# Optimization experiments

Measured on AMD Instinct MI355X. Metric: run time of the kernel, lower is better.

The kernel has to match this reference:

```python
import jax, jax.numpy as jnp
import numpy as np

DIM = 2048
N_HEAD = 16
HEAD_DIM = DIM // N_HEAD


def setup_inputs() -> dict:
    key = jax.random.key(0)
    ks = jax.random.split(key, 7)
    B, N = 2, 2048
    s = 1.0 / np.sqrt(DIM)
    return {
        "x": jax.random.normal(ks[0], (B, N, DIM), dtype=jnp.float32),
        "Wq": jax.random.normal(ks[1], (DIM, DIM), dtype=jnp.float32) * s,
        "bq": jnp.zeros((DIM,), dtype=jnp.float32),
        "Wkv": jax.random.normal(ks[2], (DIM, 2 * HEAD_DIM), dtype=jnp.float32) * s,
        "bkv": jnp.zeros((2 * HEAD_DIM,), dtype=jnp.float32),
        "Wo": jax.random.normal(ks[3], (DIM, DIM), dtype=jnp.float32) * s,
        "bo": jnp.zeros((DIM,), dtype=jnp.float32),
    }


def reference(x, Wq, bq, Wkv, bkv, Wo, bo):
    B, N, D = x.shape
    # Q projection -> (B, H, N, hd)
    q = (x @ Wq + bq).reshape(B, N, N_HEAD, HEAD_DIM).transpose(0, 2, 1, 3)
    # shared single-head K/V (kv = x, self-attention path)
    kvp = x @ Wkv + bkv  # (B, M, 2*hd)
    k, v = kvp[..., :HEAD_DIM], kvp[..., HEAD_DIM:]  # (B, M, hd) each
    scale = 1.0 / np.sqrt(HEAD_DIM).astype(np.float32)
    # broadcast shared K over heads without materializing expanded K/V
    scores = jnp.einsum("bhnd,bmd->bhnm", q, k) * scale  # (B, H, N, M)
    attn = jax.nn.softmax(scores, axis=-1)
    out = jnp.einsum("bhnm,bmd->bhnd", attn, v)  # (B, H, N, hd)
    out = out.transpose(0, 2, 1, 3).reshape(B, N, D)
    return out @ Wo + bo
```

## Files before the change

### kernel.cpp

```cpp
#include <hip/hip_runtime.h>
#include <math.h>

using bf16x8 = __attribute__((ext_vector_type(8))) short;
using f32x4  = __attribute__((ext_vector_type(4))) float;
using f32x16 = __attribute__((ext_vector_type(16))) float;
using u16x4  = __attribute__((ext_vector_type(4))) unsigned short;
using u32x4  = __attribute__((ext_vector_type(4))) unsigned int;

#define DIMSZ 2048
#define NSEQ  2048
#define BATCH 2
#define NHEAD 16
#define HD    128

__device__ __forceinline__ unsigned short f2bf(float x) {
    unsigned int u = __builtin_bit_cast(unsigned int, x);
    unsigned int r = (u + 0x7FFFu + ((u >> 16) & 1u)) >> 16;
    return (unsigned short)r;
}

__device__ __forceinline__ unsigned int cvtpk_bf16(float lo, float hi) {
    unsigned int r;
    asm("v_cvt_pk_bf16_f32 %0, %1, %2" : "=v"(r) : "v"(lo), "v"(hi));
    return r;
}

__device__ __forceinline__ void gload_lds16(const unsigned short* g, unsigned short* l) {
    __builtin_amdgcn_global_load_lds(
        (const __attribute__((address_space(1))) unsigned int*)g,
        (__attribute__((address_space(3))) unsigned int*)l, 16, 0, 0);
}

__global__ void k_cast_bf16(const float* __restrict__ in, unsigned short* __restrict__ out, int n4) {
    int i = blockIdx.x * blockDim.x + threadIdx.x;
    if (i >= n4) return;
    f32x4 v = *(const f32x4*)(in + (size_t)i * 4);
    u16x4 o;
#pragma unroll
    for (int j = 0; j < 4; j++) o[j] = f2bf(v[j]);
    *(u16x4*)(out + (size_t)i * 4) = o;
}

__global__ void k_transpose_w(const float* __restrict__ W, unsigned short* __restrict__ WT,
                              int K, int N, float scale) {
    __shared__ float t[32][33];
    int k0 = blockIdx.y * 32, n0 = blockIdx.x * 32;
    int tx = threadIdx.x, ty = threadIdx.y;
#pragma unroll
    for (int i = 0; i < 32; i += 8) t[ty + i][tx] = W[(size_t)(k0 + ty + i) * N + n0 + tx];
    __syncthreads();
#pragma unroll
    for (int i = 0; i < 32; i += 8) WT[(size_t)(n0 + ty + i) * K + k0 + tx] = f2bf(t[tx][ty + i] * scale);
}

__global__ void k_transpose_v(const unsigned short* __restrict__ kvp, unsigned short* __restrict__ vt) {
    __shared__ unsigned short t[32][33];
    int n0 = blockIdx.x * 32, d0 = blockIdx.y * 32, b = blockIdx.z;
    int tx = threadIdx.x, ty = threadIdx.y;
#pragma unroll
    for (int i = 0; i < 32; i += 8)
        t[ty + i][tx] = kvp[(size_t)(b * NSEQ + n0 + ty + i) * 256 + 128 + d0 + tx];
    __syncthreads();
#pragma unroll
    for (int i = 0; i < 32; i += 8)
        vt[(size_t)(b * HD + d0 + ty + i) * NSEQ + n0 + tx] = t[tx][ty + i];
}

__global__ __launch_bounds__(256, 2)
void k_gemm_qkv(const unsigned short* __restrict__ A, const unsigned short* __restrict__ Bt,
                const float* __restrict__ bq, float bscale, const float* __restrict__ bkv,
                unsigned short* __restrict__ qout, unsigned short* __restrict__ kvout,
                int M, int K) {
    __shared__ unsigned short As[128 * 32];
    __shared__ unsigned short Bs[128 * 32];
    const int tid = threadIdx.x;
    const int wid = tid >> 6;
    const int lane = tid & 63;
    const int g = lane >> 4, cc = lane & 15;
    const int wr = wid >> 1, wc = wid & 1;
    const size_t m0 = (size_t)blockIdx.y * 128;
    const size_t n0 = (size_t)blockIdx.x * 128;

    f32x4 acc[4][4] = {};

    const int srow = wid * 32 + (lane >> 2);
    const int sch = lane & 3;
    const unsigned short* gA = A + (m0 + srow) * (size_t)K + sch * 8;
    const unsigned short* gB = Bt + (n0 + srow) * (size_t)K + sch * 8;
    unsigned short* lA = As + wid * 32 * 32;
    unsigned short* lB = Bs + wid * 32 * 32;

    for (int k0 = 0; k0 < K; k0 += 32) {
        gload_lds16(gA + k0, lA);
        gload_lds16(gA + 16 * (size_t)K + k0, lA + 16 * 32);
        gload_lds16(gB + k0, lB);
        gload_lds16(gB + 16 * (size_t)K + k0, lB + 16 * 32);
        __syncthreads();
        bf16x8 af[4], bfr[4];
#pragma unroll
        for (int mi = 0; mi < 4; mi++) af[mi] = *(const bf16x8*)(As + (wr * 64 + mi * 16 + cc) * 32 + g * 8);
#pragma unroll
        for (int ni = 0; ni < 4; ni++) bfr[ni] = *(const bf16x8*)(Bs + (wc * 64 + ni * 16 + cc) * 32 + g * 8);
#pragma unroll
        for (int mi = 0; mi < 4; mi++)
#pragma unroll
            for (int ni = 0; ni < 4; ni++)
                acc[mi][ni] = __builtin_amdgcn_mfma_f32_16x16x32_bf16(af[mi], bfr[ni], acc[mi][ni], 0, 0, 0);
        __syncthreads();
    }

    const bool isQ = (n0 < 2048);
    const int colg = (int)n0 + wc * 64 + cc;
    const int col0 = isQ ? colg : colg - 2048;
    const int ostride = isQ ? 2048 : 256;
    unsigned short* outp = isQ ? qout : kvout;
    float bia[4];
#pragma unroll
    for (int ni = 0; ni < 4; ni++)
        bia[ni] = isQ ? bq[col0 + ni * 16] * bscale : bkv[col0 + ni * 16];
#pragma unroll
    for (int mi = 0; mi < 4; mi++) {
        size_t row = m0 + wr * 64 + mi * 16 + g * 4;
#pragma unroll
        for (int ni = 0; ni < 4; ni++)
#pragma unroll
            for (int r = 0; r < 4; r++)
                outp[(row + r) * ostride + col0 + ni * 16] = f2bf(acc[mi][ni][r] + bia[ni]);
    }
}

__global__ __launch_bounds__(256, 2)
void k_gemm_bt_f32(const unsigned short* __restrict__ A, const unsigned short* __restrict__ Bt,
                   const float* __restrict__ bias, float* __restrict__ Cout,
                   int M, int N, int K) {
    __shared__ unsigned short As[128 * 32];
    __shared__ unsigned short Bs[128 * 32];
    const int tid = threadIdx.x;
    const int wid = tid >> 6;
    const int lane = tid & 63;
    const int g = lane >> 4, cc = lane & 15;
    const int wr = wid >> 1, wc = wid & 1;
    const size_t m0 = (size_t)blockIdx.y * 128;
    const size_t n0 = (size_t)blockIdx.x * 128;

    f32x4 acc[4][4] = {};

    const int srow = wid * 32 + (lane >> 2);
    const int sch = lane & 3;
    const unsigned short* gA = A + (m0 + srow) * (size_t)K + sch * 8;
    const unsigned short* gB = Bt + (n0 + srow) * (size_t)K + sch * 8;
    unsigned short* lA = As + wid * 32 * 32;
    unsigned short* lB = Bs + wid * 32 * 32;

    for (int k0 = 0; k0 < K; k0 += 32) {
        gload_lds16(gA + k0, lA);
        gload_lds16(gA + 16 * (size_t)K + k0, lA + 16 * 32);
        gload_lds16(gB + k0, lB);
        gload_lds16(gB + 16 * (size_t)K + k0, lB + 16 * 32);
        __syncthreads();
        bf16x8 af[4], bfr[4];
#pragma unroll
        for (int mi = 0; mi < 4; mi++) af[mi] = *(const bf16x8*)(As + (wr * 64 + mi * 16 + cc) * 32 + g * 8);
#pragma unroll
        for (int ni = 0; ni < 4; ni++) bfr[ni] = *(const bf16x8*)(Bs + (wc * 64 + ni * 16 + cc) * 32 + g * 8);
#pragma unroll
        for (int mi = 0; mi < 4; mi++)
#pragma unroll
            for (int ni = 0; ni < 4; ni++)
                acc[mi][ni] = __builtin_amdgcn_mfma_f32_16x16x32_bf16(af[mi], bfr[ni], acc[mi][ni], 0, 0, 0);
        __syncthreads();
    }

    const int col0 = (int)n0 + wc * 64 + cc;
    float bia[4];
#pragma unroll
    for (int ni = 0; ni < 4; ni++) bia[ni] = bias[col0 + ni * 16];
#pragma unroll
    for (int mi = 0; mi < 4; mi++) {
        size_t row = m0 + wr * 64 + mi * 16 + g * 4;
#pragma unroll
        for (int ni = 0; ni < 4; ni++)
#pragma unroll
            for (int r = 0; r < 4; r++)
                Cout[(row + r) * N + col0 + ni * 16] = acc[mi][ni][r] + bia[ni];
    }
}

__global__ __launch_bounds__(256, 2)
void k_attn(const unsigned short* __restrict__ q, const unsigned short* __restrict__ kvp,
            const unsigned short* __restrict__ vt, unsigned short* __restrict__ out) {
    __shared__ unsigned char Kb[2][16384];
    __shared__ unsigned char Vb[2][16384];

    const int b = blockIdx.z, h = blockIdx.y, qt = blockIdx.x;
    const int tid = threadIdx.x, w = tid >> 6, lane = tid & 63;
    const int q32 = lane & 31, hi = lane >> 5;

    const int qrow = qt * 128 + w * 32 + q32;
    const unsigned short* qp = q + (size_t)(b * NSEQ + qrow) * DIMSZ + h * HD + hi * 8;
    bf16x8 qf[8];
#pragma unroll
    for (int dc = 0; dc < 8; dc++) qf[dc] = *(const bf16x8*)(qp + dc * 16);

    const char* kvpc = (const char*)kvp;
    const char* vtc  = (const char*)vt;
    size_t srcK[4], srcV[4];
#pragma unroll
    for (int c = 0; c < 4; c++) {
        unsigned int o = (tid + c * 256) * 16;
        unsigned int krow = o >> 8, kcol = o & 255;
        srcK[c] = (size_t)(b * NSEQ + krow) * 512 + (kcol ^ (((krow >> 1) & 15) << 4));
        unsigned int vrow = o >> 7, vcol = o & 127;
        srcV[c] = (size_t)(b * HD + vrow) * 4096 + (vcol ^ (((vrow >> 2) & 7) << 4));
    }

    auto STAGE = [&](int buf, int t) {
        size_t kb_ = (size_t)t * 32768;
        size_t vb_ = (size_t)t * 128;
#pragma unroll
        for (int c = 0; c < 4; c++) {
            gload_lds16((const unsigned short*)(kvpc + srcK[c] + kb_),
                        (unsigned short*)(Kb[buf] + (w * 64 + c * 256) * 16));
            gload_lds16((const unsigned short*)(vtc + srcV[c] + vb_),
                        (unsigned short*)(Vb[buf] + (w * 64 + c * 256) * 16));
        }
    };

    f32x16 o0 = {}, o1 = {}, o2 = {}, o3 = {};
    float l_run = 0.0f;
    const unsigned int swK = ((q32 >> 1) & 15) << 4;
    const unsigned int swV = ((q32 >> 2) & 7) << 4;

#define PROC_KT(S, KTB)                                                               \
    {                                                                                 \
        float pz[16];                                                                 \
        _Pragma("unroll") for (int r = 0; r < 16; r++) {                              \
            pz[r] = exp2f(S[r]);                                                      \
            l_run += pz[r];                                                           \
        }                                                                             \
        _Pragma("unroll") for (int kc = 0; kc < 2; kc++) {                            \
            unsigned int own01 = cvtpk_bf16(pz[kc * 8 + 0], pz[kc * 8 + 1]);          \
            unsigned int own23 = cvtpk_bf16(pz[kc * 8 + 2], pz[kc * 8 + 3]);          \
            unsigned int own45 = cvtpk_bf16(pz[kc * 8 + 4], pz[kc * 8 + 5]);          \
            unsigned int own67 = cvtpk_bf16(pz[kc * 8 + 6], pz[kc * 8 + 7]);          \
            unsigned int send_a = hi ? own01 : own45;                                 \
            unsigned int send_b = hi ? own23 : own67;                                 \
            unsigned int got_a = (unsigned int)__shfl_xor((int)send_a, 32, 64);       \
            unsigned int got_b = (unsigned int)__shfl_xor((int)send_b, 32, 64);       \
            u32x4 awv;                                                                \
            awv[0] = hi ? got_a : own01;                                              \
            awv[1] = hi ? got_b : own23;                                              \
            awv[2] = hi ? own45 : got_a;                                              \
            awv[3] = hi ? own67 : got_b;                                              \
            bf16x8 pa = __builtin_bit_cast(bf16x8, awv);                              \
            const unsigned int kbo = (KTB) + kc * 32 + hi * 16;                       \
            bf16x8 vf0 = *(const bf16x8*)(Vc + (q32 + 0) * 128 + (kbo ^ swV));        \
            o0 = __builtin_amdgcn_mfma_f32_32x32x16_bf16(pa, vf0, o0, 0, 0, 0);       \
            bf16x8 vf1 = *(const bf16x8*)(Vc + (q32 + 32) * 128 + (kbo ^ swV));       \
            o1 = __builtin_amdgcn_mfma_f32_32x32x16_bf16(pa, vf1, o1, 0, 0, 0);       \
            bf16x8 vf2 = *(const bf16x8*)(Vc + (q32 + 64) * 128 + (kbo ^ swV));       \
            o2 = __builtin_amdgcn_mfma_f32_32x32x16_bf16(pa, vf2, o2, 0, 0, 0);       \
            bf16x8 vf3 = *(const bf16x8*)(Vc + (q32 + 96) * 128 + (kbo ^ swV));       \
            o3 = __builtin_amdgcn_mfma_f32_32x32x16_bf16(pa, vf3, o3, 0, 0, 0);       \
        }                                                                             \
    }

    STAGE(0, 0);
    __syncthreads();

    for (int t = 0; t < NSEQ / 64; t++) {
        const int cur = t & 1;
        if (t < NSEQ / 64 - 1) STAGE(cur ^ 1, t + 1);

        const unsigned char* Kc = Kb[cur];
        const unsigned char* Vc = Vb[cur];

        f32x16 s0 = {}, s1 = {};
#pragma unroll
        for (int dc = 0; dc < 8; dc++) {
            const unsigned int db = dc * 32 + hi * 16;
            bf16x8 kf0 = *(const bf16x8*)(Kc + q32 * 256 + (db ^ swK));
            bf16x8 kf1 = *(const bf16x8*)(Kc + (q32 + 32) * 256 + (db ^ swK));
            s0 = __builtin_amdgcn_mfma_f32_32x32x16_bf16(kf0, qf[dc], s0, 0, 0, 0);
            s1 = __builtin_amdgcn_mfma_f32_32x32x16_bf16(kf1, qf[dc], s1, 0, 0, 0);
        }

        PROC_KT(s0, 0)
        PROC_KT(s1, 64)

        __syncthreads();
    }
#undef PROC_KT

    l_run += __shfl_xor(l_run, 32, 64);
    float* Lp = (float*)(Kb[0] + w * 128);
    if (hi == 0) Lp[q32] = l_run;

    float rinv[16];
#pragma unroll
    for (int r = 0; r < 16; r++) {
        int qloc = (r & 3) + 8 * (r >> 2) + 4 * hi;
        rinv[r] = 1.0f / Lp[qloc];
    }

    unsigned short* op = out + (size_t)(b * NSEQ + qt * 128 + w * 32) * DIMSZ + h * HD + q32;
#pragma unroll
    for (int r = 0; r < 16; r++) {
        int qloc = (r & 3) + 8 * (r >> 2) + 4 * hi;
        op[(size_t)qloc * DIMSZ + 0]  = f2bf(o0[r] * rinv[r]);
        op[(size_t)qloc * DIMSZ + 32] = f2bf(o1[r] * rinv[r]);
        op[(size_t)qloc * DIMSZ + 64] = f2bf(o2[r] * rinv[r]);
        op[(size_t)qloc * DIMSZ + 96] = f2bf(o3[r] * rinv[r]);
    }
}

extern "C" void kernel_launch(void* const* d_in, const int* in_sizes, int n_in,
                              void* d_out, int out_size, void* d_ws, size_t ws_size,
                              hipStream_t stream) {
    const float* x   = (const float*)d_in[0];
    const float* Wq  = (const float*)d_in[1];
    const float* bq  = (const float*)d_in[2];
    const float* Wkv = (const float*)d_in[3];
    const float* bkv = (const float*)d_in[4];
    const float* Wo  = (const float*)d_in[5];
    const float* bo  = (const float*)d_in[6];

    char* w = (char*)d_ws;
    unsigned short* xb    = (unsigned short*)(w);
    unsigned short* wqkvt = (unsigned short*)(w + 16777216);
    unsigned short* wot   = (unsigned short*)(w + 26214400);
    unsigned short* qb    = (unsigned short*)(w + 34603008);
    unsigned short* kvpb  = (unsigned short*)(w + 51380224);
    unsigned short* vtb   = (unsigned short*)(w + 53477376);
    unsigned short* aob   = xb;

    const float sc = 0.08838834764831845f * 1.4426950408889634f;

    k_cast_bf16<<<dim3((BATCH * NSEQ * DIMSZ / 4 + 255) / 256), dim3(256), 0, stream>>>(
        x, xb, BATCH * NSEQ * DIMSZ / 4);
    k_transpose_w<<<dim3(DIMSZ / 32, DIMSZ / 32), dim3(32, 8), 0, stream>>>(Wq, wqkvt, DIMSZ, DIMSZ, sc);
    k_transpose_w<<<dim3(256 / 32, DIMSZ / 32), dim3(32, 8), 0, stream>>>(
        Wkv, wqkvt + (size_t)2048 * 2048, DIMSZ, 256, 1.0f);
    k_transpose_w<<<dim3(DIMSZ / 32, DIMSZ / 32), dim3(32, 8), 0, stream>>>(Wo, wot, DIMSZ, DIMSZ, 1.0f);

    k_gemm_qkv<<<dim3(2304 / 128, BATCH * NSEQ / 128), dim3(256), 0, stream>>>(
        xb, wqkvt, bq, sc, bkv, qb, kvpb, BATCH * NSEQ, DIMSZ);
    k_transpose_v<<<dim3(NSEQ / 32, HD / 32, BATCH), dim3(32, 8), 0, stream>>>(kvpb, vtb);
    k_attn<<<dim3(NSEQ / 128, NHEAD, BATCH), dim3(256), 0, stream>>>(qb, kvpb, vtb, aob);
    k_gemm_bt_f32<<<dim3(DIMSZ / 128, BATCH * NSEQ / 128), dim3(256), 0, stream>>>(
        aob, wot, bo, (float*)d_out, BATCH * NSEQ, DIMSZ, DIMSZ);
}
```

Baseline: 218.5 us.

## Double-buffer LDS in projection GEMMs and raise MFMA priority in attention

Both projection GEMM kernels now use two LDS buffers and prefetch the next K-slice while computing the current one. This removes one barrier per iteration and lets global-to-LDS loads overlap with MFMA work. In the attention kernel, the V fragment loads are grouped ahead of the MFMAs, and the MFMA groups are wrapped in s_setprio to favour matrix issue across waves. The cost is doubled LDS use in the GEMMs, which may hurt the 2-blocks-per-CU occupancy target, plus extra register pressure from holding four V fragments at once.

```diff
diff --git a/kernel.cpp b/kernel.cpp
--- a/kernel.cpp
+++ b/kernel.cpp
@@ -71,8 +71,8 @@
                 const float* __restrict__ bq, float bscale, const float* __restrict__ bkv,
                 unsigned short* __restrict__ qout, unsigned short* __restrict__ kvout,
                 int M, int K) {
-    __shared__ unsigned short As[128 * 32];
-    __shared__ unsigned short Bs[128 * 32];
+    __shared__ unsigned short As[2][128 * 32];
+    __shared__ unsigned short Bs[2][128 * 32];
     const int tid = threadIdx.x;
     const int wid = tid >> 6;
     const int lane = tid & 63;
@@ -87,26 +87,32 @@
     const int sch = lane & 3;
     const unsigned short* gA = A + (m0 + srow) * (size_t)K + sch * 8;
     const unsigned short* gB = Bt + (n0 + srow) * (size_t)K + sch * 8;
-    unsigned short* lA = As + wid * 32 * 32;
-    unsigned short* lB = Bs + wid * 32 * 32;
-
+    const int lo = wid * 32 * 32;
+
+    auto STAGE = [&](int buf, int k0) {
+        gload_lds16(gA + k0, &As[buf][lo]);
+        gload_lds16(gA + 16 * (size_t)K + k0, &As[buf][lo + 16 * 32]);
+        gload_lds16(gB + k0, &Bs[buf][lo]);
+        gload_lds16(gB + 16 * (size_t)K + k0, &Bs[buf][lo + 16 * 32]);
+    };
+
+    STAGE(0, 0);
+    __syncthreads();
+    int cur = 0;
     for (int k0 = 0; k0 < K; k0 += 32) {
-        gload_lds16(gA + k0, lA);
-        gload_lds16(gA + 16 * (size_t)K + k0, lA + 16 * 32);
-        gload_lds16(gB + k0, lB);
-        gload_lds16(gB + 16 * (size_t)K + k0, lB + 16 * 32);
-        __syncthreads();
+        if (k0 + 32 < K) STAGE(cur ^ 1, k0 + 32);
         bf16x8 af[4], bfr[4];
 #pragma unroll
-        for (int mi = 0; mi < 4; mi++) af[mi] = *(const bf16x8*)(As + (wr * 64 + mi * 16 + cc) * 32 + g * 8);
-#pragma unroll
-        for (int ni = 0; ni < 4; ni++) bfr[ni] = *(const bf16x8*)(Bs + (wc * 64 + ni * 16 + cc) * 32 + g * 8);
+        for (int mi = 0; mi < 4; mi++) af[mi] = *(const bf16x8*)(&As[cur][(wr * 64 + mi * 16 + cc) * 32 + g * 8]);
+#pragma unroll
+        for (int ni = 0; ni < 4; ni++) bfr[ni] = *(const bf16x8*)(&Bs[cur][(wc * 64 + ni * 16 + cc) * 32 + g * 8]);
 #pragma unroll
         for (int mi = 0; mi < 4; mi++)
 #pragma unroll
             for (int ni = 0; ni < 4; ni++)
                 acc[mi][ni] = __builtin_amdgcn_mfma_f32_16x16x32_bf16(af[mi], bfr[ni], acc[mi][ni], 0, 0, 0);
         __syncthreads();
+        cur ^= 1;
     }
 
     const bool isQ = (n0 < 2048);
@@ -133,8 +139,8 @@
 void k_gemm_bt_f32(const unsigned short* __restrict__ A, const unsigned short* __restrict__ Bt,
                    const float* __restrict__ bias, float* __restrict__ Cout,
                    int M, int N, int K) {
-    __shared__ unsigned short As[128 * 32];
-    __shared__ unsigned short Bs[128 * 32];
+    __shared__ unsigned short As[2][128 * 32];
+    __shared__ unsigned short Bs[2][128 * 32];
     const int tid = threadIdx.x;
     const int wid = tid >> 6;
     const int lane = tid & 63;
@@ -149,26 +155,32 @@
     const int sch = lane & 3;
     const unsigned short* gA = A + (m0 + srow) * (size_t)K + sch * 8;
     const unsigned short* gB = Bt + (n0 + srow) * (size_t)K + sch * 8;
-    unsigned short* lA = As + wid * 32 * 32;
-    unsigned short* lB = Bs + wid * 32 * 32;
-
+    const int lo = wid * 32 * 32;
+
+    auto STAGE = [&](int buf, int k0) {
+        gload_lds16(gA + k0, &As[buf][lo]);
+        gload_lds16(gA + 16 * (size_t)K + k0, &As[buf][lo + 16 * 32]);
+        gload_lds16(gB + k0, &Bs[buf][lo]);
+        gload_lds16(gB + 16 * (size_t)K + k0, &Bs[buf][lo + 16 * 32]);
+    };
+
+    STAGE(0, 0);
+    __syncthreads();
+    int cur = 0;
     for (int k0 = 0; k0 < K; k0 += 32) {
-        gload_lds16(gA + k0, lA);
-        gload_lds16(gA + 16 * (size_t)K + k0, lA + 16 * 32);
-        gload_lds16(gB + k0, lB);
-        gload_lds16(gB + 16 * (size_t)K + k0, lB + 16 * 32);
-        __syncthreads();
+        if (k0 + 32 < K) STAGE(cur ^ 1, k0 + 32);
         bf16x8 af[4], bfr[4];
 #pragma unroll
-        for (int mi = 0; mi < 4; mi++) af[mi] = *(const bf16x8*)(As + (wr * 64 + mi * 16 + cc) * 32 + g * 8);
-#pragma unroll
-        for (int ni = 0; ni < 4; ni++) bfr[ni] = *(const bf16x8*)(Bs + (wc * 64 + ni * 16 + cc) * 32 + g * 8);
+        for (int mi = 0; mi < 4; mi++) af[mi] = *(const bf16x8*)(&As[cur][(wr * 64 + mi * 16 + cc) * 32 + g * 8]);
+#pragma unroll
+        for (int ni = 0; ni < 4; ni++) bfr[ni] = *(const bf16x8*)(&Bs[cur][(wc * 64 + ni * 16 + cc) * 32 + g * 8]);
 #pragma unroll
         for (int mi = 0; mi < 4; mi++)
 #pragma unroll
             for (int ni = 0; ni < 4; ni++)
                 acc[mi][ni] = __builtin_amdgcn_mfma_f32_16x16x32_bf16(af[mi], bfr[ni], acc[mi][ni], 0, 0, 0);
         __syncthreads();
+        cur ^= 1;
     }
 
     const int col0 = (int)n0 + wc * 64 + cc;
@@ -255,13 +267,15 @@
             bf16x8 pa = __builtin_bit_cast(bf16x8, awv);                              \
             const unsigned int kbo = (KTB) + kc * 32 + hi * 16;                       \
             bf16x8 vf0 = *(const bf16x8*)(Vc + (q32 + 0) * 128 + (kbo ^ swV));        \
+            bf16x8 vf1 = *(const bf16x8*)(Vc + (q32 + 32) * 128 + (kbo ^ swV));       \
+            bf16x8 vf2 = *(const bf16x8*)(Vc + (q32 + 64) * 128 + (kbo ^ swV));       \
+            bf16x8 vf3 = *(const bf16x8*)(Vc + (q32 + 96) * 128 + (kbo ^ swV));       \
+            __builtin_amdgcn_s_setprio(1);                                            \
             o0 = __builtin_amdgcn_mfma_f32_32x32x16_bf16(pa, vf0, o0, 0, 0, 0);       \
-            bf16x8 vf1 = *(const bf16x8*)(Vc + (q32 + 32) * 128 + (kbo ^ swV));       \
             o1 = __builtin_amdgcn_mfma_f32_32x32x16_bf16(pa, vf1, o1, 0, 0, 0);       \
-            bf16x8 vf2 = *(const bf16x8*)(Vc + (q32 + 64) * 128 + (kbo ^ swV));       \
             o2 = __builtin_amdgcn_mfma_f32_32x32x16_bf16(pa, vf2, o2, 0, 0, 0);       \
-            bf16x8 vf3 = *(const bf16x8*)(Vc + (q32 + 96) * 128 + (kbo ^ swV));       \
             o3 = __builtin_amdgcn_mfma_f32_32x32x16_bf16(pa, vf3, o3, 0, 0, 0);       \
+            __builtin_amdgcn_s_setprio(0);                                            \
         }                                                                             \
     }
 
@@ -281,8 +295,10 @@
             const unsigned int db = dc * 32 + hi * 16;
             bf16x8 kf0 = *(const bf16x8*)(Kc + q32 * 256 + (db ^ swK));
             bf16x8 kf1 = *(const bf16x8*)(Kc + (q32 + 32) * 256 + (db ^ swK));
+            __builtin_amdgcn_s_setprio(1);
             s0 = __builtin_amdgcn_mfma_f32_32x32x16_bf16(kf0, qf[dc], s0, 0, 0, 0);
             s1 = __builtin_amdgcn_mfma_f32_32x32x16_bf16(kf1, qf[dc], s1, 0, 0, 0);
+            __builtin_amdgcn_s_setprio(0);
         }
 
         PROC_KT(s0, 0)
```

Result: no change. 218.6 us (+0.1%).
